# Kernel tuning notes

Measured on AMD Instinct MI355X. Metric: run time of the kernel, lower is better.

Reference implementation:

```python
import jax, jax.numpy as jnp
import numpy as np

H = 256      # GRU hidden size
E = 768      # embedding_len
H2 = 2 * H   # bidirectional feature dim
NL, NR = 2, 2
DE = (NL + NR) * H2
B, LF = 16, 32


def setup_inputs() -> dict:
    key = jax.random.key(0)
    it = iter(jax.random.split(key, 32))
    def rn(shape, s=0.05):
        return jax.random.normal(next(it), shape, jnp.float32) * s
    return {
        "left_f0": rn((B, LF, E), 1.0),
        "left_f1": rn((B, LF, E), 1.0),
        "right_f0": rn((B, LF, E), 1.0),
        "right_f1": rn((B, LF, E), 1.0),
        "gru_Wih0": rn((2, 3 * H, E)),
        "gru_Whh0": rn((2, 3 * H, H)),
        "gru_bih0": jnp.zeros((2, 3 * H), jnp.float32),
        "gru_bhh0": jnp.zeros((2, 3 * H), jnp.float32),
        "gru_Wih12": rn((2, 2, 3 * H, H2)),
        "gru_Whh12": rn((2, 2, 3 * H, H)),
        "gru_bih12": jnp.zeros((2, 2, 3 * H), jnp.float32),
        "gru_bhh12": jnp.zeros((2, 2, 3 * H), jnp.float32),
        "hwt_Wn": rn((H2, H2)), "hwt_bn": jnp.zeros((H2,), jnp.float32),
        "hwt_Wg": rn((H2, H2)), "hwt_bg": jnp.full((H2,), -2.0, jnp.float32),
        "lint_W": rn((1, H2)), "lint_b": jnp.zeros((1,), jnp.float32),
        "attr_left": rn((NL, H2)), "attr_right": rn((NR, H2)),
        "empty_attr": rn((H2,)),
        "hwe_Wn": rn((DE, DE)), "hwe_bn": jnp.zeros((DE,), jnp.float32),
        "hwe_Wg": rn((DE, DE)), "hwe_bg": jnp.full((DE,), -2.0, jnp.float32),
        "line_W": rn((2, DE)),
        "line_b": jnp.full((2,), float(-np.log(0.99 / 0.01)), jnp.float32),
    }


def _gru_layer(x, Wih, Whh, bih, bhh, reverse):
    # x: [B,T,D] -> [B,T,H], PyTorch GRU gate order (r, z, n)
    xi = jnp.einsum('btd,gd->btg', x, Wih) + bih
    xi = jnp.swapaxes(xi, 0, 1)  # [T,B,3H]
    h0 = jnp.zeros((x.shape[0], H), x.dtype)
    def step(h, xt):
        gh = h @ Whh.T + bhh
        ir, iz, inn = jnp.split(xt, 3, axis=-1)
        hr, hz, hn = jnp.split(gh, 3, axis=-1)
        r = jax.nn.sigmoid(ir + hr)
        z = jax.nn.sigmoid(iz + hz)
        n = jnp.tanh(inn + r * hn)
        h_new = (1 - z) * n + z * h
        return h_new, h_new
    _, ys = jax.lax.scan(step, h0, xi, reverse=reverse)
    return jnp.swapaxes(ys, 0, 1)


def _masked_softmax(x, mask, axis):
    return jax.nn.softmax(x + jnp.where(mask, 0.0, -1e10), axis=axis)


def _highway(x, Wn, bn, Wg, bg):
    n = jax.nn.relu(x @ Wn.T + bn)
    g = jax.nn.sigmoid(x @ Wg.T + bg)
    return n * g + (1 - g) * x


def reference(left_f0, left_f1, right_f0, right_f1,
              gru_Wih0, gru_Whh0, gru_bih0, gru_bhh0,
              gru_Wih12, gru_Whh12, gru_bih12, gru_bhh12,
              hwt_Wn, hwt_bn, hwt_Wg, hwt_bg, lint_W, lint_b,
              attr_left, attr_right, empty_attr,
              hwe_Wn, hwe_bn, hwe_Wg, hwe_bg, line_W, line_b):
    def bigru(x):
        f = _gru_layer(x, gru_Wih0[0], gru_Whh0[0], gru_bih0[0], gru_bhh0[0], False)
        b = _gru_layer(x, gru_Wih0[1], gru_Whh0[1], gru_bih0[1], gru_bhh0[1], True)
        h = jnp.concatenate([f, b], -1)
        for l in range(2):
            f = _gru_layer(h, gru_Wih12[l, 0], gru_Whh12[l, 0], gru_bih12[l, 0], gru_bhh12[l, 0], False)
            b = _gru_layer(h, gru_Wih12[l, 1], gru_Whh12[l, 1], gru_bih12[l, 1], gru_bhh12[l, 1], True)
            h = jnp.concatenate([f, b], -1)
        return h  # [B,T,2H]

    left_fields = [left_f0, left_f1]
    right_fields = [right_f0, right_f1]
    left_emb = [bigru(v) for v in left_fields]
    right_emb = [bigru(v) for v in right_fields]

    def masks(fields):
        tm = [jnp.sum(v != 0, axis=2) > 0 for v in fields]
        am = [jnp.sum(m, axis=1, keepdims=True) > 0 for m in tm]
        return jnp.concatenate(tm, 1), jnp.concatenate(am, 1)

    l_tok_mask, l_attr_mask = masks(left_fields)
    r_tok_mask, r_attr_mask = masks(right_fields)

    def token_matching(Le, Re, r_mask):
        L = jnp.concatenate(Le, 1)
        R = jnp.concatenate(Re, 1)
        cm = jnp.abs(L[:, :, None, :] - R[:, None, :, :])   # [B,L,R,2H]
        hw = _highway(cm, hwt_Wn, hwt_bn, hwt_Wg, hwt_bg)
        scores = hw @ lint_W.T + lint_b                     # [B,L,R,1]
        w = _masked_softmax(scores, r_mask[:, None, :, None], axis=2)
        return jnp.sum(cm * w, axis=2)                      # [B,L,2H]

    l_cmp = token_matching(left_emb, right_emb, r_tok_mask)
    r_cmp = token_matching(right_emb, left_emb, l_tok_mask)

    def attribute_matching(embs, attr_emb, cmp_res, tok_mask, attr_mask):
        start, res = 0, []
        for i, v in enumerate(embs):
            Lf = v.shape[1]
            m = tok_mask[:, start:start + Lf]               # [B,Lf]
            w = _masked_softmax(v @ attr_emb[i], m, axis=1)[:, :, None]
            res.append(jnp.sum(cmp_res[:, start:start + Lf] * w, axis=1))
            start += Lf
        res = jnp.stack(res, axis=1)                        # [B,nf,2H]
        return jnp.where(attr_mask[:, :, None], res, empty_attr)

    l_rep = attribute_matching(left_emb, attr_left, l_cmp, l_tok_mask, l_attr_mask)
    r_rep = attribute_matching(right_emb, attr_right, r_cmp, r_tok_mask, r_attr_mask)

    concat = jnp.concatenate([l_rep, r_rep], axis=1).reshape(l_rep.shape[0], -1)
    hw = _highway(concat, hwe_Wn, hwe_bn, hwe_Wg, hwe_bg)
    out = hw @ line_W.T + line_b
    return jax.nn.log_softmax(out, axis=1)
```

## Files before the change

kernel.cpp:

```cpp
#include <hip/hip_runtime.h>
#include <hip/hip_bf16.h>

#define NH 256
#define NE 768
#define NH2 512
#define NG3 768
#define NB 16
#define NLF 32
#define NBT 2048
#define NDE 2048

typedef short s16x8 __attribute__((ext_vector_type(8)));
typedef float f32x4 __attribute__((ext_vector_type(4)));

#define TK_SWZ(g, r) (((g) + ((r) >> 1)) & 3)

#if __has_builtin(__builtin_amdgcn_global_load_lds)
#define GLOAD_LDS16(gp, lp) \
  __builtin_amdgcn_global_load_lds((const __attribute__((address_space(1))) unsigned int*)(gp), \
                                   (__attribute__((address_space(3))) unsigned int*)(lp), 16, 0, 0)
#define HAVE_GLLDS 1
#else
#define HAVE_GLLDS 0
#endif

__device__ __forceinline__ float fsig_(float x){
  return __builtin_amdgcn_rcpf(1.f + __expf(-x));
}
__device__ __forceinline__ float ftanh_(float x){
  float e = __expf(2.f*x);
  return 1.f - 2.f*__builtin_amdgcn_rcpf(e + 1.f);
}
__device__ __forceinline__ unsigned short f2bf_(float f){
  unsigned int x = __float_as_uint(f);
  unsigned int r = (x + 0x7fffu + ((x>>16)&1u)) >> 16;
  return (unsigned short)r;
}
__device__ __forceinline__ float bfx_(unsigned int u){ return __uint_as_float(u << 16); }
__device__ __forceinline__ unsigned int pack_bf16_rnd(float a, float b){
  unsigned int ua = __float_as_uint(a) + 0x8000u;
  unsigned int ub = __float_as_uint(b) + 0x8000u;
  return __builtin_amdgcn_perm(ub, ua, 0x07060302u);
}
__device__ __forceinline__ int tokrow(int side, int b, int tok){
  return (((side*2 + (tok>>5))*16 + b) << 5) + (tok & 31);
}
__device__ __forceinline__ float xiget_(const uint4* x4, int idx){
  const unsigned int* w = (const unsigned int*)x4;
  unsigned int v = w[idx >> 1];
  return (idx & 1) ? __uint_as_float(v & 0xffff0000u) : __uint_as_float(v << 16);
}

__global__ void k_gather(const float* __restrict__ f0, const float* __restrict__ f1,
                         const float* __restrict__ f2, const float* __restrict__ f3,
                         float* __restrict__ X0){
  int m = blockIdx.x;
  int f = m >> 9, rem = m & 511;
  const float* src = (f==0)? f0 : (f==1)? f1 : (f==2)? f2 : f3;
  const float* sp = src + (size_t)rem*NE;
  float* dp = X0 + (size_t)m*NE;
  for (int d = threadIdx.x; d < NE; d += 256) dp[d] = sp[d];
}

__global__ void k_masks(const float* __restrict__ f0, const float* __restrict__ f1,
                        const float* __restrict__ f2, const float* __restrict__ f3,
                        float* __restrict__ TM, float* __restrict__ AM){
  int f = blockIdx.x, b = blockIdx.y;
  const float* src = (f==0)? f0 : (f==1)? f1 : (f==2)? f2 : f3;
  __shared__ unsigned int flags[33];
  if (threadIdx.x < 33) flags[threadIdx.x] = 0u;
  __syncthreads();
  for (int t = 0; t < 32; t++){
    const float* row = src + ((size_t)b*NLF + t)*NE;
    bool nz = false;
    for (int d = threadIdx.x; d < NE; d += 256) nz |= (row[d] != 0.f);
    if (nz) atomicOr(&flags[t], 1u);
  }
  __syncthreads();
  int side = f >> 1, fi = f & 1;
  if (threadIdx.x < 32){
    unsigned int fl = flags[threadIdx.x];
    TM[side*1024 + b*64 + fi*32 + threadIdx.x] = fl ? 1.f : 0.f;
    if (fl) atomicOr(&flags[32], 1u);
  }
  __syncthreads();
  if (threadIdx.x == 0) AM[side*32 + b*2 + fi] = flags[32] ? 1.f : 0.f;
}

__global__ void k_prep_whh(const float* __restrict__ w0, const float* __restrict__ w12,
                           unsigned short* __restrict__ dst){
  int idx = blockIdx.x*256 + threadIdx.x;
  float v = (idx < 393216) ? w0[idx] : w12[idx - 393216];
  dst[idx] = f2bf_(v);
}

__global__ void k_prep_tw(const float* __restrict__ Wn, const float* __restrict__ Wg,
                          unsigned short* __restrict__ TW){
  int idx = blockIdx.x*256 + threadIdx.x;
  int kpos = idx & 31;
  int n    = (idx >> 5) & 127;
  int kc   = (idx >> 12) & 15;
  int nc   = idx >> 16;
  int gpos = kpos >> 3, j = kpos & 7;
  int gorig = (gpos - (n>>1)) & 3;
  int k = kc*32 + gorig*8 + j;
  int q = n >> 1, type = n & 1;
  const float* src = type ? Wg : Wn;
  TW[idx] = f2bf_(src[(size_t)(nc*64 + q)*NH2 + k]);
}

template<bool ABF16>
__global__ __launch_bounds__(256) void k_gemm_mfma(
    const void* __restrict__ Av,
    const float* __restrict__ Wb, long wsz,
    const float* __restrict__ biasb, long bsz,
    unsigned short* __restrict__ XIo, long csz,
    int K)
{
  int z = blockIdx.z;
  const float* W = Wb + (size_t)z*wsz;
  const float* bias = biasb + (size_t)z*bsz;
  unsigned short* XO = XIo + (size_t)z*csz;
  int n0 = blockIdx.x*128, m0 = blockIdx.y*128;
  __shared__ short At[128*32];
  __shared__ short Wt[128*32];
  int tid = threadIdx.x;
  int wave = tid >> 6, wm = wave >> 1, wn = wave & 1;
  int lane = tid & 63, l15 = lane & 15, lq = lane >> 4;
  int sm = tid & 127, gb = (tid >> 7) * 2;

  f32x4 zero4 = {0.f,0.f,0.f,0.f};
  f32x4 acc[4][4];
  #pragma unroll
  for (int mi=0;mi<4;mi++)
    #pragma unroll
    for (int nj=0;nj<4;nj++) acc[mi][nj] = zero4;

  const float* wr = W + (size_t)(n0 + sm)*K;

  for (int k0 = 0; k0 < K; k0 += 32){
    if constexpr (ABF16){
      const unsigned short* ar = (const unsigned short*)Av + (size_t)(m0 + sm)*K;
      #pragma unroll
      for (int gi = 0; gi < 2; gi++){
        int g = gb + gi;
        *(uint4*)&At[sm*32 + TK_SWZ(g,sm)*8] = *(const uint4*)&ar[k0 + g*8];
      }
    } else {
      const float* ar = (const float*)Av + (size_t)(m0 + sm)*K;
      #pragma unroll
      for (int gi = 0; gi < 2; gi++){
        int g = gb + gi;
        const float* ap = ar + k0 + g*8;
        float4 a0 = *(const float4*)ap, a1 = *(const float4*)(ap+4);
        uint4 pa = { pack_bf16_rnd(a0.x,a0.y), pack_bf16_rnd(a0.z,a0.w),
                     pack_bf16_rnd(a1.x,a1.y), pack_bf16_rnd(a1.z,a1.w) };
        *(uint4*)&At[sm*32 + TK_SWZ(g,sm)*8] = pa;
      }
    }
    #pragma unroll
    for (int gi = 0; gi < 2; gi++){
      int g = gb + gi;
      const float* wp = wr + k0 + g*8;
      float4 w0 = *(const float4*)wp, w1 = *(const float4*)(wp+4);
      uint4 pw = { pack_bf16_rnd(w0.x,w0.y), pack_bf16_rnd(w0.z,w0.w),
                   pack_bf16_rnd(w1.x,w1.y), pack_bf16_rnd(w1.z,w1.w) };
      *(uint4*)&Wt[sm*32 + TK_SWZ(g,sm)*8] = pw;
    }
    __syncthreads();
    s16x8 af[4], wf[4];
    #pragma unroll
    for (int mi=0;mi<4;mi++){
      int row = wm*64 + mi*16 + l15;
      af[mi] = *(const s16x8*)&At[row*32 + TK_SWZ(lq,row)*8];
    }
    #pragma unroll
    for (int nj=0;nj<4;nj++){
      int row = wn*64 + nj*16 + l15;
      wf[nj] = *(const s16x8*)&Wt[row*32 + TK_SWZ(lq,row)*8];
    }
    #pragma unroll
    for (int mi=0;mi<4;mi++)
      #pragma unroll
      for (int nj=0;nj<4;nj++)
        acc[mi][nj] = __builtin_amdgcn_mfma_f32_16x16x32_bf16(af[mi], wf[nj], acc[mi][nj], 0,0,0);
    __syncthreads();
  }
  #pragma unroll
  for (int nj=0;nj<4;nj++){
    int n = n0 + wn*64 + nj*16 + l15;
    float bv = bias[n];
    int gg = n >> 8;
    int u256 = n & 255;
    int p = u256 >> 7, w_s = (u256 >> 4) & 7, l15_s = u256 & 15;
    int cofs = (p*3 + gg)*4;
    #pragma unroll
    for (int mi=0;mi<4;mi++){
      int mbase = m0 + wm*64 + mi*16 + lq*4;
      int t0 = mbase & 31, bp = mbase >> 5;
      int g = bp >> 4, mloc = bp & 15;
      int lq_s = mloc >> 2, r4 = mloc & 3;
      int tid_s = w_s*64 + lq_s*16 + l15_s;
      size_t base = ((size_t)(t0*4 + g)*512 + tid_s)*24 + cofs + r4;
      #pragma unroll
      for (int r=0;r<4;r++)
        XO[base + (size_t)r*49152] = f2bf_(acc[mi][nj][r] + bv);
    }
  }
}

__global__ __launch_bounds__(512, 2) void k_scan_mfma(
    const unsigned short* __restrict__ xi,
    const unsigned short* __restrict__ whh,
    const float* __restrict__ bhhb, long bhh_stride,
    unsigned short* __restrict__ Hout,
    int chain0)
{
  int g = blockIdx.x;
  int dir = blockIdx.y;
  int tid = threadIdx.x;
  int w = tid >> 6;
  int lane = tid & 63, l15 = lane & 15, lq = lane >> 4;
  const unsigned short* W = whh + (size_t)(chain0 + dir)*NG3*NH;
  const float* bhh = bhhb + (size_t)dir*bhh_stride;
  const unsigned short* xid = xi + (size_t)dir*1572864;
  int b0 = g*16;

  __shared__ unsigned short hbuf[2*16*264];
  for (int i = tid; i < 2*16*264; i += 512) hbuf[i] = 0;

  uint4 xc4[3], xn4[3];
  {
    int t0 = dir ? 31 : 0;
    const uint4* p0 = (const uint4*)(xid + ((size_t)(t0*4 + g)*512 + tid)*24);
    xc4[0] = p0[0]; xc4[1] = p0[1]; xc4[2] = p0[2];
  }

  s16x8 warr[6][8];
  #pragma unroll
  for (int p6 = 0; p6 < 6; p6++){
    const unsigned short* wp = W + (size_t)(16*(w + 8*p6) + l15)*NH + lq*8;
    #pragma unroll
    for (int kt = 0; kt < 8; kt++)
      warr[p6][kt] = *(const s16x8*)(wp + kt*32);
  }
  float brv[2], bzv[2], bnv[2];
  #pragma unroll
  for (int p = 0; p < 2; p++){
    int u = p*128 + 16*w + l15;
    brv[p] = bhh[u]; bzv[p] = bhh[256+u]; bnv[p] = bhh[512+u];
  }
  float hreg[2][4] = {{0,0,0,0},{0,0,0,0}};
  __syncthreads();

  for (int s = 0; s < 32; s++){
    int t = dir ? (31 - s) : s;
    int cur = s & 1, nxt = cur ^ 1;
    const unsigned short* rbp = hbuf + cur*4224;
    unsigned short* wbp = hbuf + nxt*4224;

    if (s < 31){
      int tn = dir ? (31 - (s+1)) : (s+1);
      const uint4* pn = (const uint4*)(xid + ((size_t)(tn*4 + g)*512 + tid)*24);
      xn4[0] = pn[0]; xn4[1] = pn[1]; xn4[2] = pn[2];
    }

    f32x4 acc[6];
    #pragma unroll
    for (int p6 = 0; p6 < 6; p6++) acc[p6] = (f32x4){0.f,0.f,0.f,0.f};
    #pragma unroll
    for (int kt = 0; kt < 8; kt++){
      s16x8 a = *(const s16x8*)&rbp[l15*264 + kt*32 + lq*8];
      #pragma unroll
      for (int p6 = 0; p6 < 6; p6++)
        acc[p6] = __builtin_amdgcn_mfma_f32_16x16x32_bf16(a, warr[p6][kt], acc[p6], 0,0,0);
    }

    #pragma unroll
    for (int p = 0; p < 2; p++){
      int u = p*128 + 16*w + l15;
      #pragma unroll
      for (int r4 = 0; r4 < 4; r4++){
        int m = lq*4 + r4;
        float xr_ = xiget_(xc4, (p*3+0)*4 + r4);
        float xz_ = xiget_(xc4, (p*3+1)*4 + r4);
        float xn_ = xiget_(xc4, (p*3+2)*4 + r4);
        float rr = fsig_(xr_ + acc[p][r4]   + brv[p]);
        float zz = fsig_(xz_ + acc[2+p][r4] + bzv[p]);
        float nn = ftanh_(xn_ + rr*(acc[4+p][r4] + bnv[p]));
        float hnew = (1.f - zz)*nn + zz*hreg[p][r4];
        hreg[p][r4] = hnew;
        unsigned short hb = f2bf_(hnew);
        wbp[m*264 + u] = hb;
        Hout[((size_t)(b0 + m)*32 + t)*NH2 + dir*256 + u] = hb;
      }
    }
    if (s < 31){
      xc4[0] = xn4[0]; xc4[1] = xn4[1]; xc4[2] = xn4[2];
    }
    __syncthreads();
  }
}

__global__ __launch_bounds__(256) void k_cm_pretile(
    const unsigned short* __restrict__ Hf, unsigned short* __restrict__ CMT, int b0)
{
  int ip = blockIdx.x, bl = blockIdx.y;
  int b = b0 + bl;
  int tid = threadIdx.x;
  int m = tid & 127, gb = (tid >> 7) * 2;
  int i_ = ip*2 + (m >> 6), j_ = m & 63;
  const unsigned short* Lrow = Hf + (size_t)tokrow(0, b, i_)*NH2;
  const unsigned short* Rrow = Hf + (size_t)tokrow(1, b, j_)*NH2;
  unsigned short* dst = CMT + ((size_t)(bl*32 + ip) * 16) * 4096;
  for (int kc = 0; kc < 16; kc++){
    int k0 = kc*32;
    #pragma unroll
    for (int gi = 0; gi < 2; gi++){
      int g = gb + gi;
      uint4 lu = *(const uint4*)&Lrow[k0 + g*8];
      uint4 ru = *(const uint4*)&Rrow[k0 + g*8];
      unsigned int lw[4] = {lu.x, lu.y, lu.z, lu.w};
      unsigned int rw[4] = {ru.x, ru.y, ru.z, ru.w};
      uint4 pk;
      unsigned int pr[4];
      #pragma unroll
      for (int q = 0; q < 4; q++){
        float la = __uint_as_float(lw[q] << 16), lb = __uint_as_float(lw[q] & 0xffff0000u);
        float ra = __uint_as_float(rw[q] << 16), rb = __uint_as_float(rw[q] & 0xffff0000u);
        pr[q] = pack_bf16_rnd(fabsf(la - ra), fabsf(lb - rb));
      }
      pk.x = pr[0]; pk.y = pr[1]; pk.z = pr[2]; pk.w = pr[3];
      *(uint4*)&dst[kc*4096 + m*32 + TK_SWZ(g,m)*8] = pk;
    }
  }
}

__global__ __launch_bounds__(256) void k_token_mfma(
    const unsigned short* __restrict__ CMT,
    const unsigned short* __restrict__ TW,
    const float* __restrict__ bn, const float* __restrict__ bg,
    const float* __restrict__ lintW,
    float* __restrict__ P, int b0)
{
  __shared__ short Atile[4096];
  __shared__ short Btile[4096];
  __shared__ short Asave[8192];
  __shared__ float sred[256];
  int ip = blockIdx.x, bl = blockIdx.y, nc = blockIdx.z;
  int b = b0 + bl;
  int tid = threadIdx.x;
  int wave = tid >> 6, wm = wave >> 1, wn = wave & 1;
  int lane = tid & 63, l15 = lane & 15, lq = lane >> 4;

  const char* Ab = (const char*)(CMT + ((size_t)(bl*32 + ip) * 16) * 4096);
  const char* Bb = (const char*)(TW + ((size_t)(nc*16)) * 4096);

  f32x4 zero4 = {0.f,0.f,0.f,0.f};
  f32x4 acc[4][4];
  #pragma unroll
  for (int mi=0;mi<4;mi++)
    #pragma unroll
    for (int nj=0;nj<4;nj++) acc[mi][nj] = zero4;

  for (int kc = 0; kc < 16; kc++){
    const char* gA = Ab + (size_t)kc*8192;
    const char* gB = Bb + (size_t)kc*8192;
#if HAVE_GLLDS
    char* lA = (char*)Atile + wave*1024;
    char* lB = (char*)Btile + wave*1024;
    GLOAD_LDS16(gA + tid*16, lA);
    GLOAD_LDS16(gA + 4096 + tid*16, lA + 4096);
    GLOAD_LDS16(gB + tid*16, lB);
    GLOAD_LDS16(gB + 4096 + tid*16, lB + 4096);
    int cs = kc - 2*nc;
    if ((unsigned)cs < 2u){
      char* lS = (char*)Asave + cs*8192 + wave*1024;
      GLOAD_LDS16(gA + tid*16, lS);
      GLOAD_LDS16(gA + 4096 + tid*16, lS + 4096);
    }
#else
    {
      uint4 va0 = ((const uint4*)gA)[tid], va1 = ((const uint4*)gA)[256+tid];
      uint4 vb0 = ((const uint4*)gB)[tid], vb1 = ((const uint4*)gB)[256+tid];
      ((uint4*)Atile)[tid] = va0; ((uint4*)Atile)[256+tid] = va1;
      ((uint4*)Btile)[tid] = vb0; ((uint4*)Btile)[256+tid] = vb1;
      int cs = kc - 2*nc;
      if ((unsigned)cs < 2u){
        ((uint4*)Asave)[cs*512 + tid] = va0; ((uint4*)Asave)[cs*512 + 256+tid] = va1;
      }
    }
#endif
    __syncthreads();
    s16x8 af[4], bfv[4];
    #pragma unroll
    for (int mi=0;mi<4;mi++){
      int row = wm*64 + mi*16 + l15;
      af[mi] = *(const s16x8*)&Atile[row*32 + TK_SWZ(lq,row)*8];
    }
    #pragma unroll
    for (int nj=0;nj<4;nj++){
      int row = wn*64 + nj*16 + l15;
      bfv[nj] = *(const s16x8*)&Btile[row*32 + TK_SWZ(lq,row)*8];
    }
    #pragma unroll
    for (int mi=0;mi<4;mi++)
      #pragma unroll
      for (int nj=0;nj<4;nj++)
        acc[mi][nj] = __builtin_amdgcn_mfma_f32_16x16x32_bf16(af[mi], bfv[nj], acc[mi][nj], 0,0,0);
    __syncthreads();
  }

  float bnv[4], bgv[4], lwv[4]; int qv[4];
  #pragma unroll
  for (int nj=0;nj<4;nj++){
    int q = (wn*64 + nj*16 + l15) >> 1;
    qv[nj] = q;
    int nf = nc*64 + q;
    bnv[nj] = bn[nf]; bgv[nj] = bg[nf]; lwv[nj] = lintW[nf];
  }
  float lmask = (l15 & 1) ? 0.f : 1.f;
  float sc[4][4];
  #pragma unroll
  for (int mi=0;mi<4;mi++)
    #pragma unroll
    for (int r=0;r<4;r++) sc[mi][r] = 0.f;

  #pragma unroll
  for (int nj=0;nj<4;nj++){
    int q = qv[nj];
    int cs = q >> 5, kk = q & 31, gor = kk >> 3, el = kk & 7;
    #pragma unroll
    for (int mi=0;mi<4;mi++){
      int mbase = wm*64 + mi*16 + lq*4;
      #pragma unroll
      for (int r=0;r<4;r++){
        float v  = acc[mi][nj][r];
        float pv = __shfl_xor(v, 1);
        int mm = mbase + r;
        unsigned short cu = (unsigned short)Asave[cs*4096 + mm*32 + TK_SWZ(gor,mm)*8 + el];
        float cmf = __uint_as_float(((unsigned int)cu) << 16);
        float an = v + bnv[nj];
        float gg = fsig_(pv + bgv[nj]);
        float hw = fmaxf(an, 0.f)*gg + (1.f - gg)*cmf;
        sc[mi][r] += lmask * lwv[nj] * hw;
      }
    }
  }
  #pragma unroll
  for (int mi=0;mi<4;mi++)
    #pragma unroll
    for (int r=0;r<4;r++){
      float v = sc[mi][r];
      v += __shfl_xor(v, 1); v += __shfl_xor(v, 2);
      v += __shfl_xor(v, 4); v += __shfl_xor(v, 8);
      sc[mi][r] = v;
    }
  if (l15 == 0){
    #pragma unroll
    for (int mi=0;mi<4;mi++)
      #pragma unroll
      for (int r=0;r<4;r++)
        sred[(wm*64 + mi*16 + lq*4 + r)*2 + wn] = sc[mi][r];
  }
  __syncthreads();
  if (tid < 128){
    float v = sred[tid*2] + sred[tid*2+1];
    int isel = tid >> 6, j = tid & 63;
    P[(((size_t)nc*16 + b)*64 + (ip*2 + isel))*64 + j] = v;
  }
}

__global__ void k_score_reduce(const float* __restrict__ P, float* __restrict__ S){
  int idx = blockIdx.x*256 + threadIdx.x;
  float v = 0.f;
  #pragma unroll
  for (int nc = 0; nc < 8; nc++) v += P[(size_t)nc*65536 + idx];
  S[idx] = v;
}

__global__ void k_softmax_wl(const float* __restrict__ S, const float* __restrict__ TM,
                             float* __restrict__ WLo){
  int i = blockIdx.x, b = blockIdx.y, j = threadIdx.x;
  float mask = TM[1024 + b*64 + j];
  float v = S[((size_t)b*64 + i)*64 + j] + (mask != 0.f ? 0.f : -1e10f);
  float m = v;
  for (int o = 32; o; o >>= 1) m = fmaxf(m, __shfl_xor(m, o));
  float e = __expf(v - m), s = e;
  for (int o = 32; o; o >>= 1) s += __shfl_xor(s, o);
  WLo[((size_t)b*64 + i)*64 + j] = e / s;
}
__global__ void k_softmax_wr(const float* __restrict__ S, const float* __restrict__ TM,
                             float* __restrict__ WRo){
  int j = blockIdx.x, b = blockIdx.y, i = threadIdx.x;
  float mask = TM[b*64 + i];
  float v = S[((size_t)b*64 + i)*64 + j] + (mask != 0.f ? 0.f : -1e10f);
  float m = v;
  for (int o = 32; o; o >>= 1) m = fmaxf(m, __shfl_xor(m, o));
  float e = __expf(v - m), s = e;
  for (int o = 32; o; o >>= 1) s += __shfl_xor(s, o);
  WRo[((size_t)b*64 + j)*64 + i] = e / s;
}

__global__ __launch_bounds__(256) void k_cmp(const unsigned short* __restrict__ Hf,
    const float* __restrict__ w, float* __restrict__ out, int side){
  int p = blockIdx.x, b = blockIdx.y;
  __shared__ float wl[64];
  if (threadIdx.x < 64) wl[threadIdx.x] = w[((size_t)b*64 + p)*64 + threadIdx.x];
  __syncthreads();
  int xr = tokrow(side, b, p);
  int d1 = threadIdx.x, d2 = threadIdx.x + 256;
  float x1 = bfx_(Hf[(size_t)xr*NH2 + d1]), x2 = bfx_(Hf[(size_t)xr*NH2 + d2]);
  float a1 = 0.f, a2 = 0.f;
  for (int q = 0; q < 64; q++){
    const unsigned short* yr = Hf + (size_t)tokrow(side^1, b, q)*NH2;
    float wq = wl[q];
    a1 += wq * fabsf(x1 - bfx_(yr[d1]));
    a2 += wq * fabsf(x2 - bfx_(yr[d2]));
  }
  out[((size_t)b*64 + p)*NH2 + d1] = a1;
  out[((size_t)b*64 + p)*NH2 + d2] = a2;
}

__global__ __launch_bounds__(256) void k_attr(const unsigned short* __restrict__ Hf,
    const float* __restrict__ attrL, const float* __restrict__ attrR,
    const float* __restrict__ LC, const float* __restrict__ RC,
    const float* __restrict__ TM, const float* __restrict__ AM,
    const float* __restrict__ emptyA, float* __restrict__ CC){
  int fi = blockIdx.x, b = blockIdx.y, side = blockIdx.z;
  const float* attr = (side ? attrR : attrL) + fi*512;
  const float* cmp = side ? RC : LC;
  __shared__ float sc[32], wv[32];
  int t = threadIdx.x >> 3, l8 = threadIdx.x & 7;
  const unsigned short* er = Hf + (size_t)tokrow(side, b, fi*32 + t)*NH2;
  float acc = 0.f;
  for (int d = l8*64; d < l8*64 + 64; d++) acc += bfx_(er[d])*attr[d];
  acc += __shfl_down(acc, 4, 8);
  acc += __shfl_down(acc, 2, 8);
  acc += __shfl_down(acc, 1, 8);
  if (l8 == 0) sc[t] = acc;
  __syncthreads();
  if (threadIdx.x < 32){
    float mask = TM[side*1024 + b*64 + fi*32 + threadIdx.x];
    float v = sc[threadIdx.x] + (mask != 0.f ? 0.f : -1e10f);
    float m = v;
    for (int o = 16; o; o >>= 1) m = fmaxf(m, __shfl_xor(m, o, 32));
    float e = __expf(v - m), s = e;
    for (int o = 16; o; o >>= 1) s += __shfl_xor(s, o, 32);
    wv[threadIdx.x] = e / s;
  }
  __syncthreads();
  float am = AM[side*32 + b*2 + fi];
  int d1 = threadIdx.x, d2 = threadIdx.x + 256;
  float a1 = 0.f, a2 = 0.f;
  for (int t2 = 0; t2 < 32; t2++){
    float wq = wv[t2];
    const float* cr = cmp + ((size_t)b*64 + fi*32 + t2)*NH2;
    a1 += wq * cr[d1];
    a2 += wq * cr[d2];
  }
  float* dst = CC + (size_t)b*NDE + (size_t)(side*2 + fi)*512;
  dst[d1] = (am != 0.f) ? a1 : emptyA[d1];
  dst[d2] = (am != 0.f) ? a2 : emptyA[d2];
}

__global__ __launch_bounds__(256) void k_final_hw(const float* __restrict__ X,
    const float* __restrict__ Wn, const float* __restrict__ bn,
    const float* __restrict__ Wg, const float* __restrict__ bg,
    float* __restrict__ HWo){
  __shared__ float Xs[4][2048];
  int nb = blockIdx.x, bq = blockIdx.y;
  for (int idx = threadIdx.x; idx < 8192; idx += 256)
    Xs[idx>>11][idx & 2047] = X[(size_t)(bq*4 + (idx>>11))*NDE + (idx & 2047)];
  __syncthreads();
  int nl = threadIdx.x >> 1, kl = threadIdx.x & 1;
  int n = nb*128 + nl;
  const float* wnr = Wn + (size_t)n*NDE + kl*1024;
  const float* wgr = Wg + (size_t)n*NDE + kl*1024;
  float an[4] = {0,0,0,0}, ag[4] = {0,0,0,0};
  for (int k = 0; k < 1024; k++){
    float wn = wnr[k], wg = wgr[k];
    int kk = kl*1024 + k;
    #pragma unroll
    for (int b4 = 0; b4 < 4; b4++){
      float xv = Xs[b4][kk];
      an[b4] = fmaf(wn, xv, an[b4]);
      ag[b4] = fmaf(wg, xv, ag[b4]);
    }
  }
  #pragma unroll
  for (int b4 = 0; b4 < 4; b4++){
    an[b4] += __shfl_down(an[b4], 1);
    ag[b4] += __shfl_down(ag[b4], 1);
  }
  if (kl == 0){
    float bnv = bn[n], bgv = bg[n];
    #pragma unroll
    for (int b4 = 0; b4 < 4; b4++){
      float a = an[b4] + bnv;
      float g = fsig_(ag[b4] + bgv);
      float xv = Xs[b4][n];
      HWo[(size_t)(bq*4 + b4)*NDE + n] = fmaxf(a, 0.f)*g + (1.f - g)*xv;
    }
  }
}

__global__ void k_out(const float* __restrict__ HWi, const float* __restrict__ lw,
                      const float* __restrict__ lb, float* __restrict__ out){
  int b = blockIdx.x, lane = threadIdx.x;
  float p0 = 0.f, p1 = 0.f;
  for (int n = lane; n < 2048; n += 64){
    float h = HWi[(size_t)b*NDE + n];
    p0 += h * lw[n];
    p1 += h * lw[2048 + n];
  }
  for (int o = 32; o; o >>= 1){ p0 += __shfl_xor(p0, o); p1 += __shfl_xor(p1, o); }
  if (lane == 0){
    float o0 = p0 + lb[0], o1 = p1 + lb[1];
    float m = fmaxf(o0, o1);
    float lse = m + logf(expf(o0 - m) + expf(o1 - m));
    out[b*2]   = o0 - lse;
    out[b*2+1] = o1 - lse;
  }
}

extern "C" void kernel_launch(void* const* d_in, const int* in_sizes, int n_in,
                              void* d_out, int out_size, void* d_ws, size_t ws_size,
                              hipStream_t stream){
  const float* lf0 = (const float*)d_in[0];
  const float* lf1 = (const float*)d_in[1];
  const float* rf0 = (const float*)d_in[2];
  const float* rf1 = (const float*)d_in[3];
  const float* gWih0 = (const float*)d_in[4];
  const float* gWhh0 = (const float*)d_in[5];
  const float* gbih0 = (const float*)d_in[6];
  const float* gbhh0 = (const float*)d_in[7];
  const float* gWih12 = (const float*)d_in[8];
  const float* gWhh12 = (const float*)d_in[9];
  const float* gbih12 = (const float*)d_in[10];
  const float* gbhh12 = (const float*)d_in[11];
  const float* hwtWn = (const float*)d_in[12];
  const float* hwtbn = (const float*)d_in[13];
  const float* hwtWg = (const float*)d_in[14];
  const float* hwtbg = (const float*)d_in[15];
  const float* lintW = (const float*)d_in[16];
  const float* attrL = (const float*)d_in[18];
  const float* attrR = (const float*)d_in[19];
  const float* emptyA = (const float*)d_in[20];
  const float* hweWn = (const float*)d_in[21];
  const float* hwebn = (const float*)d_in[22];
  const float* hweWg = (const float*)d_in[23];
  const float* hwebg = (const float*)d_in[24];
  const float* lineW = (const float*)d_in[25];
  const float* lineB = (const float*)d_in[26];
  float* out = (float*)d_out;

  unsigned short* HA = (unsigned short*)d_ws;
  unsigned short* HB = HA + 1048576;
  unsigned short* WHH = HB + 1048576;
  unsigned short* TW  = WHH + 1179648;
  float* Sb  = (float*)(TW + 524288);
  float* WLb = Sb  + 65536;
  float* WRb = WLb + 65536;
  float* LC  = WRb + 65536;
  float* RC  = LC + 524288;
  float* TM  = RC + 524288;
  float* AM  = TM + 2048;
  float* CC  = AM + 64;
  float* HWb = CC + 32768;
  float* P   = HWb + 32768;
  unsigned short* CMT = (unsigned short*)(P + 524288);
  float* X0 = (float*)CMT;
  unsigned short* XI = (unsigned short*)(X0 + 1572864);

  k_gather<<<NBT, 256, 0, stream>>>(lf0, lf1, rf0, rf1, X0);
  k_masks<<<dim3(4,16), 256, 0, stream>>>(lf0, lf1, rf0, rf1, TM, AM);
  k_prep_whh<<<4608, 256, 0, stream>>>(gWhh0, gWhh12, WHH);
  k_prep_tw<<<2048, 256, 0, stream>>>(hwtWn, hwtWg, TW);

  const long XSZ = 1572864;
  k_gemm_mfma<false><<<dim3(6,16,2), 256, 0, stream>>>(X0, gWih0, (long)NG3*NE, gbih0, NG3,
                                                       XI, XSZ, NE);
  k_scan_mfma<<<dim3(4,2), 512, 0, stream>>>(XI, WHH, gbhh0, NG3, HA, 0);
  k_gemm_mfma<true><<<dim3(6,16,2), 256, 0, stream>>>(HA, gWih12, (long)NG3*NH2, gbih12, NG3,
                                                      XI, XSZ, NH2);
  k_scan_mfma<<<dim3(4,2), 512, 0, stream>>>(XI, WHH, gbhh12, NG3, HB, 2);
  k_gemm_mfma<true><<<dim3(6,16,2), 256, 0, stream>>>(HB, gWih12 + (size_t)2*NG3*NH2, (long)NG3*NH2,
                                                      gbih12 + 2*NG3, NG3,
                                                      XI, XSZ, NH2);
  k_scan_mfma<<<dim3(4,2), 512, 0, stream>>>(XI, WHH, gbhh12 + 2*NG3, NG3, HA, 4);

  for (int c = 0; c < 4; c++){
    k_cm_pretile<<<dim3(32,4), 256, 0, stream>>>(HA, CMT, c*4);
    k_token_mfma<<<dim3(32,4,8), 256, 0, stream>>>(CMT, TW, hwtbn, hwtbg, lintW, P, c*4);
  }
  k_score_reduce<<<256, 256, 0, stream>>>(P, Sb);
  k_softmax_wl<<<dim3(64,16), 64, 0, stream>>>(Sb, TM, WLb);
  k_softmax_wr<<<dim3(64,16), 64, 0, stream>>>(Sb, TM, WRb);
  k_cmp<<<dim3(64,16), 256, 0, stream>>>(HA, WLb, LC, 0);
  k_cmp<<<dim3(64,16), 256, 0, stream>>>(HA, WRb, RC, 1);

  k_attr<<<dim3(2,16,2), 256, 0, stream>>>(HA, attrL, attrR, LC, RC, TM, AM, emptyA, CC);

  k_final_hw<<<dim3(16,4), 256, 0, stream>>>(CC, hweWn, hwebn, hweWg, hwebg, HWb);
  k_out<<<16, 64, 0, stream>>>(HWb, lineW, lineB, out);
}
```

Baseline: 809.9 us.

## Replace scalar final highway GEMV with split-K bf16 MFMA GEMM plus reduce

The final 2048x2048 highway layer used a scalar FMA kernel launched on only 64 blocks. It now runs as a bf16 MFMA GEMM over 256 blocks, split four ways along K and between the two weight matrices, writing partial sums into a scratch buffer. A separate elementwise kernel then reduces the partials and applies the bias, sigmoid gate and ReLU. The goal is more parallelism across CUs and matrix-core throughput on this weight-bandwidth-bound stage. In exchange, weights and activations are rounded to bf16 on load, and the extra launch and partial-sum traffic add cost.

```diff
diff --git a/kernel.cpp b/kernel.cpp
--- a/kernel.cpp
+++ b/kernel.cpp
@@ -564,45 +564,67 @@
   dst[d2] = (am != 0.f) ? a2 : emptyA[d2];
 }
 
-__global__ __launch_bounds__(256) void k_final_hw(const float* __restrict__ X,
-    const float* __restrict__ Wn, const float* __restrict__ bn,
-    const float* __restrict__ Wg, const float* __restrict__ bg,
+__global__ __launch_bounds__(256) void k_final_gemm(
+    const float* __restrict__ X,
+    const float* __restrict__ Wn, const float* __restrict__ Wg,
+    float* __restrict__ P2)
+{
+  int nt = blockIdx.x, ks = blockIdx.y, z = blockIdx.z;
+  const float* W = z ? Wg : Wn;
+  int n0 = nt*64, k0 = ks*512;
+  __shared__ short At[16*32];
+  __shared__ short Wt[64*32];
+  int tid = threadIdx.x;
+  int w = tid >> 6, lane = tid & 63, l15 = lane & 15, lq = lane >> 4;
+  int sm = tid & 63, gW = tid >> 6;
+  int sa = tid & 15, ga = (tid >> 4) & 3;
+
+  f32x4 acc = {0.f,0.f,0.f,0.f};
+  for (int kc = 0; kc < 16; kc++){
+    int kk = k0 + kc*32;
+    {
+      const float* wp = W + (size_t)(n0 + sm)*NDE + kk + gW*8;
+      float4 w0 = *(const float4*)wp, w1 = *(const float4*)(wp+4);
+      uint4 pw = { pack_bf16_rnd(w0.x,w0.y), pack_bf16_rnd(w0.z,w0.w),
+                   pack_bf16_rnd(w1.x,w1.y), pack_bf16_rnd(w1.z,w1.w) };
+      *(uint4*)&Wt[sm*32 + TK_SWZ(gW,sm)*8] = pw;
+    }
+    if (tid < 64){
+      const float* xp = X + (size_t)sa*NDE + kk + ga*8;
+      float4 x0 = *(const float4*)xp, x1 = *(const float4*)(xp+4);
+      uint4 pa = { pack_bf16_rnd(x0.x,x0.y), pack_bf16_rnd(x0.z,x0.w),
+                   pack_bf16_rnd(x1.x,x1.y), pack_bf16_rnd(x1.z,x1.w) };
+      *(uint4*)&At[sa*32 + TK_SWZ(ga,sa)*8] = pa;
+    }
+    __syncthreads();
+    s16x8 af = *(const s16x8*)&At[l15*32 + TK_SWZ(lq,l15)*8];
+    int row = w*16 + l15;
+    s16x8 bf = *(const s16x8*)&Wt[row*32 + TK_SWZ(lq,row)*8];
+    acc = __builtin_amdgcn_mfma_f32_16x16x32_bf16(af, bf, acc, 0,0,0);
+    __syncthreads();
+  }
+  int n = n0 + w*16 + l15;
+  #pragma unroll
+  for (int r = 0; r < 4; r++){
+    int b = lq*4 + r;
+    P2[(((size_t)z*4 + ks)*16 + b)*NDE + n] = acc[r];
+  }
+}
+
+__global__ void k_final_reduce(const float* __restrict__ P2,
+    const float* __restrict__ X, const float* __restrict__ bn, const float* __restrict__ bg,
     float* __restrict__ HWo){
-  __shared__ float Xs[4][2048];
-  int nb = blockIdx.x, bq = blockIdx.y;
-  for (int idx = threadIdx.x; idx < 8192; idx += 256)
-    Xs[idx>>11][idx & 2047] = X[(size_t)(bq*4 + (idx>>11))*NDE + (idx & 2047)];
-  __syncthreads();
-  int nl = threadIdx.x >> 1, kl = threadIdx.x & 1;
-  int n = nb*128 + nl;
-  const float* wnr = Wn + (size_t)n*NDE + kl*1024;
-  const float* wgr = Wg + (size_t)n*NDE + kl*1024;
-  float an[4] = {0,0,0,0}, ag[4] = {0,0,0,0};
-  for (int k = 0; k < 1024; k++){
-    float wn = wnr[k], wg = wgr[k];
-    int kk = kl*1024 + k;
-    #pragma unroll
-    for (int b4 = 0; b4 < 4; b4++){
-      float xv = Xs[b4][kk];
-      an[b4] = fmaf(wn, xv, an[b4]);
-      ag[b4] = fmaf(wg, xv, ag[b4]);
-    }
-  }
-  #pragma unroll
-  for (int b4 = 0; b4 < 4; b4++){
-    an[b4] += __shfl_down(an[b4], 1);
-    ag[b4] += __shfl_down(ag[b4], 1);
-  }
-  if (kl == 0){
-    float bnv = bn[n], bgv = bg[n];
-    #pragma unroll
-    for (int b4 = 0; b4 < 4; b4++){
-      float a = an[b4] + bnv;
-      float g = fsig_(ag[b4] + bgv);
-      float xv = Xs[b4][n];
-      HWo[(size_t)(bq*4 + b4)*NDE + n] = fmaxf(a, 0.f)*g + (1.f - g)*xv;
-    }
-  }
+  int idx = blockIdx.x*256 + threadIdx.x;
+  int b = idx >> 11, n = idx & 2047;
+  float an = bn[n], ag = bg[n];
+  #pragma unroll
+  for (int ks = 0; ks < 4; ks++){
+    an += P2[((size_t)(0*4 + ks)*16 + b)*NDE + n];
+    ag += P2[((size_t)(1*4 + ks)*16 + b)*NDE + n];
+  }
+  float g = fsig_(ag);
+  float x = X[(size_t)b*NDE + n];
+  HWo[(size_t)b*NDE + n] = fmaxf(an, 0.f)*g + (1.f - g)*x;
 }
 
 __global__ void k_out(const float* __restrict__ HWi, const float* __restrict__ lw,
@@ -672,6 +694,7 @@
   unsigned short* CMT = (unsigned short*)(P + 524288);
   float* X0 = (float*)CMT;
   unsigned short* XI = (unsigned short*)(X0 + 1572864);
+  float* P2 = (float*)CMT;
 
   k_gather<<<NBT, 256, 0, stream>>>(lf0, lf1, rf0, rf1, X0);
   k_masks<<<dim3(4,16), 256, 0, stream>>>(lf0, lf1, rf0, rf1, TM, AM);
@@ -702,6 +725,7 @@
 
   k_attr<<<dim3(2,16,2), 256, 0, stream>>>(HA, attrL, attrR, LC, RC, TM, AM, emptyA, CC);
 
-  k_final_hw<<<dim3(16,4), 256, 0, stream>>>(CC, hweWn, hwebn, hweWg, hwebg, HWb);
+  k_final_gemm<<<dim3(32,4,2), 256, 0, stream>>>(CC, hweWn, hweWg, P2);
+  k_final_reduce<<<128, 256, 0, stream>>>(P2, CC, hwebn, hwebg, HWb);
   k_out<<<16, 64, 0, stream>>>(HWb, lineW, lineB, out);
 }
```

Result: faster. 750.0 us (-7.4%).
